# Kernel tuning notes

Measured on AMD Instinct MI355X. Metric: run time of the kernel, lower is better.

## Reference

```python
import jax, jax.numpy as jnp
import numpy as np

HID = 256      # hard-coded hidden_size in the torch module
LEVELS = 16    # topological levels in the generated DAG


def _lstm_cell(x, h, c, Wih, Whh, bih, bhh):
    # PyTorch LSTM cell: gates ordered (input, forget, cell, output)
    g = x @ Wih.T + h @ Whh.T + bih + bhh
    i, f, gg, o = jnp.split(g, 4, axis=-1)
    c_new = jax.nn.sigmoid(f) * c + jax.nn.sigmoid(i) * jnp.tanh(gg)
    h_new = jax.nn.sigmoid(o) * jnp.tanh(c_new)
    return h_new, c_new


def _forward(tokens, parents_idx, parent_valid,
             Wih_tok, Whh_tok, bih_tok, bhh_tok,
             Wih_ins, Whh_ins, bih_ins, bhh_ins, Wlin, blin):
    N, T, E = tokens.shape
    K = N // LEVELS
    NEG = jnp.asarray(-1e30, tokens.dtype)

    # --- token-level LSTM over each instruction's tokens, batched across instrs ---
    def tok_step(carry, x):
        h, c = carry
        return _lstm_cell(x, h, c, Wih_tok, Whh_tok, bih_tok, bhh_tok), None
    z = jnp.zeros((N, HID), tokens.dtype)
    (ins_embed, _), _ = jax.lax.scan(tok_step, (z, z), tokens.transpose(1, 0, 2))
    # ins_embed: [N, HID] = final token-LSTM hidden per instruction

    # --- instruction-level LSTM over the DAG, level by level ---
    H = jnp.zeros((N, HID), tokens.dtype)
    C = jnp.zeros((N, HID), tokens.dtype)
    for l in range(LEVELS):
        sl = slice(l * K, (l + 1) * K)
        pidx = parents_idx[sl]                 # [K, P] indices into earlier levels
        pval = parent_valid[sl][..., None]     # [K, P, 1]
        ph = jnp.where(pval, H[pidx], NEG).max(axis=1)   # max-reduction combine
        pc = jnp.where(pval, C[pidx], NEG).max(axis=1)
        has = parent_valid[sl].any(axis=1, keepdims=True)
        h0 = jnp.where(has, ph, 0.0)           # no parents -> zero init_hidden
        c0 = jnp.where(has, pc, 0.0)
        h1, c1 = _lstm_cell(ins_embed[sl], h0, c0, Wih_ins, Whh_ins, bih_ins, bhh_ins)
        H = H.at[sl].set(h1)
        C = C.at[sl].set(c1)

    # roots = instructions with no children (never referenced as a parent)
    appears = jnp.zeros((N,), jnp.int32).at[parents_idx.reshape(-1)].add(
        parent_valid.reshape(-1).astype(jnp.int32))
    root = (appears == 0)[:, None]
    final = jnp.where(root, H, NEG).max(axis=0)   # [HID]
    return final @ Wlin.T + blin                   # [num_classes]


def setup_inputs() -> dict:
    N, T, E, P = 2048, 16, 512, 8
    K = N // LEVELS
    rng = np.random.default_rng(0)
    pidx = np.zeros((N, P), np.int32)
    pval = np.zeros((N, P), bool)
    for l in range(1, LEVELS):
        pidx[l * K:(l + 1) * K] = rng.integers(0, l * K, (K, P))
        pval[l * K:(l + 1) * K] = rng.random((K, P)) < 0.75
    key = jax.random.key(0)
    ks = jax.random.split(key, 6)
    s = lambda k, shape, fan: jax.random.normal(k, shape, jnp.float32) / np.float32(np.sqrt(fan))
    return {
        "tokens": jax.random.normal(ks[0], (N, T, E), jnp.float32),
        "parents_idx": jnp.asarray(pidx),
        "parent_valid": jnp.asarray(pval),
        "Wih_tok": s(ks[1], (4 * HID, E), E),
        "Whh_tok": s(ks[2], (4 * HID, HID), HID),
        "bih_tok": jnp.zeros((4 * HID,), jnp.float32),
        "bhh_tok": jnp.zeros((4 * HID,), jnp.float32),
        "Wih_ins": s(ks[3], (4 * HID, HID), HID),
        "Whh_ins": s(ks[4], (4 * HID, HID), HID),
        "bih_ins": jnp.zeros((4 * HID,), jnp.float32),
        "bhh_ins": jnp.zeros((4 * HID,), jnp.float32),
        "Wlin": s(ks[5], (1, HID), HID),
        "blin": jnp.zeros((1,), jnp.float32),
    }


def reference(tokens, parents_idx, parent_valid,
              Wih_tok, Whh_tok, bih_tok, bhh_tok,
              Wih_ins, Whh_ins, bih_ins, bhh_ins, Wlin, blin):
    return _forward(tokens, parents_idx, parent_valid,
                    Wih_tok, Whh_tok, bih_tok, bhh_tok,
                    Wih_ins, Whh_ins, bih_ins, bhh_ins, Wlin, blin)
```

## Files before the change

### kernel.cpp

```cpp
#include <hip/hip_runtime.h>

#define NTOK 2048
#define TT   16
#define EE   512
#define HIDD 256
#define G4   1024
#define NLVL 16
#define KLVL 128
#define INV2048 (1.0f/2048.0f)

typedef _Float16 v8h __attribute__((ext_vector_type(8)));
typedef _Float16 v4h __attribute__((ext_vector_type(4)));
typedef float    v4f __attribute__((ext_vector_type(4)));

__device__ __forceinline__ v4f mfma16(v8h a, v8h b, v4f c) {
  return __builtin_amdgcn_mfma_f32_16x16x32_f16(a, b, c, 0, 0, 0);
}

__device__ __forceinline__ float fsig(float x) {
  return 1.0f / (1.0f + __expf(-x));
}
__device__ __forceinline__ float ftanh(float x) {
  float ax = fabsf(x);
  float e  = __expf(-2.0f * ax);
  float t  = (1.0f - e) / (1.0f + e);
  return copysignf(t, x);
}

__device__ __forceinline__ void split8(const v4f& w0, const v4f& w1, v8h& hi, v8h& lo) {
#pragma unroll
  for (int u = 0; u < 4; ++u) {
    float v = w0[u]; _Float16 h = (_Float16)v;
    hi[u] = h; lo[u] = (_Float16)((v - (float)h) * 2048.0f);
  }
#pragma unroll
  for (int u = 0; u < 4; ++u) {
    float v = w1[u]; _Float16 h = (_Float16)v;
    hi[4+u] = h; lo[4+u] = (_Float16)((v - (float)h) * 2048.0f);
  }
}

__device__ __forceinline__ v8h cvt8(const v4f& w0, const v4f& w1) {
  v8h r;
#pragma unroll
  for (int u = 0; u < 4; ++u) { r[u] = (_Float16)w0[u]; r[4+u] = (_Float16)w1[u]; }
  return r;
}

__global__ __launch_bounds__(256) void knorm(const void* __restrict__ pv_raw,
                                             unsigned char* __restrict__ pv8) {
  __shared__ int mode;
  const int tid = threadIdx.x;
  if (tid == 0) mode = 0;
  __syncthreads();
  const unsigned* pu = (const unsigned*)pv_raw;
  int local = 0;
  for (int i = tid; i < 4096; i += 256) {
    unsigned v = pu[i];
    if (v == 0x3F800000u) { local = 2; break; }
    if (v > 1u) local = 1;
  }
  if (local) atomicMax(&mode, local);
  __syncthreads();
  const int m = mode;
  const unsigned char* pb = (const unsigned char*)pv_raw;
  const float* pf = (const float*)pv_raw;
  const int* pi = (const int*)pv_raw;
  for (int i = tid; i < NTOK * 8; i += 256) {
    unsigned char v;
    if (m == 1)      v = (pb[i] != 0);
    else if (m == 2) v = (pf[i] != 0.0f);
    else             v = (pi[i] != 0);
    pv8[i] = v;
  }
}

__global__ __launch_bounds__(256) void kw_cvt(
    const float* __restrict__ a0, _Float16* __restrict__ f0,
    const float* __restrict__ a1, _Float16* __restrict__ f1,
    const float* __restrict__ a2, _Float16* __restrict__ f2,
    const float* __restrict__ a3, _Float16* __restrict__ f3) {
  const int t = blockIdx.x * 256 + threadIdx.x;
  if (t < 32768) {
    const int row = t >> 5, col8 = (t & 31) * 8;
    const int fc = row >> 4, l15 = row & 15;
    const int kk = col8 >> 5, lq = (col8 >> 3) & 3;
    const int lane8 = (lq * 16 + l15) * 8;
    const size_t srow = (size_t)row * 256 + col8;
    {
      v4f x0 = *(const v4f*)(a0 + srow), x1 = *(const v4f*)(a0 + srow + 4);
      *(v8h*)(f0 + (size_t)(fc * 8 + kk) * 512 + lane8) = cvt8(x0, x1);
    }
    {
      v4f x0 = *(const v4f*)(a1 + srow), x1 = *(const v4f*)(a1 + srow + 4);
      v8h hi, lo; split8(x0, x1, hi, lo);
      _Float16* d = f1 + (size_t)(fc * 8 + kk) * 1024 + lane8;
      *(v8h*)d = hi; *(v8h*)(d + 512) = lo;
    }
    {
      v4f x0 = *(const v4f*)(a2 + srow), x1 = *(const v4f*)(a2 + srow + 4);
      v8h hi, lo; split8(x0, x1, hi, lo);
      _Float16* d = f2 + (size_t)(fc * 8 + kk) * 1024 + lane8;
      *(v8h*)d = hi; *(v8h*)(d + 512) = lo;
    }
  } else {
    const int k = t - 32768;
    const int row = k >> 6, col8 = (k & 63) * 8;
    const int fc = row >> 4, l15 = row & 15;
    const int kk = col8 >> 5, lq = (col8 >> 3) & 3;
    const size_t srow = (size_t)row * 512 + col8;
    v4f x0 = *(const v4f*)(a3 + srow), x1 = *(const v4f*)(a3 + srow + 4);
    *(v8h*)(f3 + (size_t)(fc * 16 + kk) * 512 + (lq * 16 + l15) * 8) = cvt8(x0, x1);
  }
}

__global__ __launch_bounds__(512, 1) void kg2(const float* __restrict__ A,
                                              const _Float16* __restrict__ WtH,
                                              const float* __restrict__ b1,
                                              const float* __restrict__ b2,
                                              _Float16* __restrict__ Xg, int h) {
  __shared__ _Float16 As[64 * 520];
  const int tid  = threadIdx.x;
  const int lane = tid & 63;
  const int nq   = tid >> 6;
  const int l15  = lane & 15;
  const int lq   = lane >> 4;
  const int m0   = blockIdx.x * 64;

#pragma unroll
  for (int p = 0; p < 4; ++p) {
    const int row  = p * 16 + (tid >> 5);
    const int col0 = (tid & 31) * 16;
    const int ar   = m0 + row;
    const int tokrow = (ar & 2047) * 16 + h * 8 + (ar >> 11);
    const float* s = A + (size_t)tokrow * EE + col0;
    v4f x0 = *(const v4f*)s, x1 = *(const v4f*)(s + 4);
    v4f x2 = *(const v4f*)(s + 8), x3 = *(const v4f*)(s + 12);
    _Float16* d = As + row * 520 + col0;
    *(v8h*)d       = cvt8(x0, x1);
    *(v8h*)(d + 8) = cvt8(x2, x3);
  }
  __syncthreads();

  v4f acc[4][8];
#pragma unroll
  for (int n = 0; n < 8; ++n) {
    const int col = (nq * 8 + n) * 16 + l15;
    const float bb = b1[col] + b2[col];
#pragma unroll
    for (int m = 0; m < 4; ++m) acc[m][n] = (v4f){bb, bb, bb, bb};
  }

#pragma unroll 4
  for (int kk = 0; kk < 16; ++kk) {
    v8h af[4];
#pragma unroll
    for (int m = 0; m < 4; ++m)
      af[m] = *(const v8h*)(As + (m * 16 + l15) * 520 + kk * 32 + lq * 8);
#pragma unroll
    for (int n = 0; n < 8; ++n) {
      const int fc = nq * 8 + n;
      v8h bh = *(const v8h*)(WtH + (size_t)(fc * 16 + kk) * 512 + lane * 8);
#pragma unroll
      for (int m = 0; m < 4; ++m) acc[m][n] = mfma16(af[m], bh, acc[m][n]);
    }
  }

#pragma unroll
  for (int m = 0; m < 4; ++m)
#pragma unroll
    for (int n = 0; n < 8; ++n) {
      const int row = m0 + m * 16 + lq * 4;
      const int col = (nq * 8 + n) * 16 + l15;
      v4h o;
#pragma unroll
      for (int r = 0; r < 4; ++r) o[r] = (_Float16)acc[m][n][r];
      *(v4h*)(Xg + ((size_t)(row >> 2) * G4 + col) * 4) = o;
    }
}

__global__ __launch_bounds__(512, 1) void kr3(const _Float16* __restrict__ Xg,
                                              const _Float16* __restrict__ WhhH,
                                              float* __restrict__ Hst,
                                              float* __restrict__ Cst,
                                              _Float16* __restrict__ emb, int q) {
  __shared__ float hbuf[2][16 * 260];
  const int tid  = threadIdx.x;
  const int lane = tid & 63;
  const int w    = tid >> 6;
  const int wv   = w & 3;
  const int jh   = w >> 2;
  const int l15  = lane & 15;
  const int lq   = lane >> 4;
  const int r0   = blockIdx.x * 16;

  const _Float16* wbase = WhhH + (size_t)(8 * jh + wv) * 4096 + lane * 8;

  v4f c[2];
  if (q) {
#pragma unroll
    for (int j2 = 0; j2 < 2; ++j2) {
      const int feat = 16 * (wv + 4 * (2 * jh + j2)) + l15;
#pragma unroll
      for (int r = 0; r < 4; ++r)
        c[j2][r] = Cst[(size_t)(r0 + lq * 4 + r) * HIDD + feat];
    }
    for (int idx = tid; idx < 4096; idx += 512)
      hbuf[0][(idx >> 8) * 260 + (idx & 255)] = Hst[(size_t)(r0 + (idx >> 8)) * HIDD + (idx & 255)];
  } else {
    c[0] = (v4f){0.f, 0.f, 0.f, 0.f};
    c[1] = (v4f){0.f, 0.f, 0.f, 0.f};
  }

  v4h xp[4][2];
  {
    const size_t xrow = (size_t)((r0 >> 2) + lq) * G4;
#pragma unroll
    for (int g = 0; g < 4; ++g)
#pragma unroll
      for (int j2 = 0; j2 < 2; ++j2) {
        const int col = 256 * g + 16 * (wv + 4 * (2 * jh + j2)) + l15;
        xp[g][j2] = *(const v4h*)(Xg + (xrow + col) * 4);
      }
  }

  v8h bA[8], bB[8];
#pragma unroll
  for (int g = 0; g < 4; ++g)
#pragma unroll
    for (int j2 = 0; j2 < 2; ++j2)
      bA[g * 2 + j2] = *(const v8h*)(wbase + (16 * g + 4 * j2) * 4096);
  __syncthreads();

#pragma unroll 1
  for (int tl = 0; tl < 8; ++tl) {
    const int cur = tl & 1;
    const bool have_h = (q > 0) || (tl > 0);
    v4f acc[4][2];
#pragma unroll
    for (int g = 0; g < 4; ++g)
#pragma unroll
      for (int j2 = 0; j2 < 2; ++j2) {
        v4f a;
#pragma unroll
        for (int r = 0; r < 4; ++r) a[r] = (float)xp[g][j2][r];
        acc[g][j2] = a;
      }
    if (tl < 7) {
      const size_t xrow = (size_t)((tl + 1) * 512 + (r0 >> 2) + lq) * G4;
#pragma unroll
      for (int g = 0; g < 4; ++g)
#pragma unroll
        for (int j2 = 0; j2 < 2; ++j2) {
          const int col = 256 * g + 16 * (wv + 4 * (2 * jh + j2)) + l15;
          xp[g][j2] = *(const v4h*)(Xg + (xrow + col) * 4);
        }
    }
    if (have_h) {
#pragma unroll
      for (int kp = 0; kp < 4; ++kp) {
        const int k0 = 2 * kp, k1 = 2 * kp + 1;
#pragma unroll
        for (int g = 0; g < 4; ++g)
#pragma unroll
          for (int j2 = 0; j2 < 2; ++j2)
            bB[g * 2 + j2] = *(const v8h*)(wbase + (16 * g + 4 * j2) * 4096 + k1 * 512);
        {
          const int ko = k0 * 32 + lq * 8;
          v4f w0 = *(const v4f*)(hbuf[cur] + l15 * 260 + ko);
          v4f w1 = *(const v4f*)(hbuf[cur] + l15 * 260 + ko + 4);
          v8h ah = cvt8(w0, w1);
#pragma unroll
          for (int g = 0; g < 4; ++g)
#pragma unroll
            for (int j2 = 0; j2 < 2; ++j2)
              acc[g][j2] = mfma16(ah, bA[g * 2 + j2], acc[g][j2]);
        }
        if (kp < 3) {
#pragma unroll
          for (int g = 0; g < 4; ++g)
#pragma unroll
            for (int j2 = 0; j2 < 2; ++j2)
              bA[g * 2 + j2] = *(const v8h*)(wbase + (16 * g + 4 * j2) * 4096 + (k1 + 1) * 512);
        }
        {
          const int ko = k1 * 32 + lq * 8;
          v4f w0 = *(const v4f*)(hbuf[cur] + l15 * 260 + ko);
          v4f w1 = *(const v4f*)(hbuf[cur] + l15 * 260 + ko + 4);
          v8h ah = cvt8(w0, w1);
#pragma unroll
          for (int g = 0; g < 4; ++g)
#pragma unroll
            for (int j2 = 0; j2 < 2; ++j2)
              acc[g][j2] = mfma16(ah, bB[g * 2 + j2], acc[g][j2]);
        }
      }
      if (tl < 7) {
#pragma unroll
        for (int g = 0; g < 4; ++g)
#pragma unroll
          for (int j2 = 0; j2 < 2; ++j2)
            bA[g * 2 + j2] = *(const v8h*)(wbase + (16 * g + 4 * j2) * 4096);
      }
    }
#pragma unroll
    for (int j2 = 0; j2 < 2; ++j2) {
      const int feat = 16 * (wv + 4 * (2 * jh + j2)) + l15;
#pragma unroll
      for (int r = 0; r < 4; ++r) {
        const int rr = lq * 4 + r;
        float cn = fsig(acc[1][j2][r]) * c[j2][r] + fsig(acc[0][j2][r]) * ftanh(acc[2][j2][r]);
        float hn = fsig(acc[3][j2][r]) * ftanh(cn);
        c[j2][r] = cn;
        hbuf[cur ^ 1][rr * 260 + feat] = hn;
        if (tl == 7) {
          const size_t grow = r0 + rr;
          if (!q) { Hst[grow * HIDD + feat] = hn; Cst[grow * HIDD + feat] = cn; }
          else    { emb[grow * HIDD + feat] = (_Float16)hn; }
        }
      }
    }
    __syncthreads();
  }
}

__global__ __launch_bounds__(256) void kapp(const int* __restrict__ pidx,
                                            const unsigned char* __restrict__ pval,
                                            int* __restrict__ appears) {
  int e = blockIdx.x * 512 + threadIdx.x * 2;
#pragma unroll
  for (int u = 0; u < 2; ++u, ++e) {
    if (pval[e]) atomicAdd(appears + pidx[e], 1);
  }
}

__global__ __launch_bounds__(256) void klevel(
    const _Float16* __restrict__ emb,
    const _Float16* __restrict__ WihF, const _Float16* __restrict__ WhhF,
    const float* __restrict__ bi, const float* __restrict__ bh,
    const int* __restrict__ pidx, const unsigned char* __restrict__ pval,
    float* __restrict__ H, float* __restrict__ C, int l) {
  __shared__ _Float16 h0s[16 * 264];
  __shared__ float    c0s[16 * 68];
  __shared__ int      pis[128];
  __shared__ unsigned char pvs[128];
  const int tid  = threadIdx.x;
  const int lane = tid & 63;
  const int wv   = tid >> 6;
  const int l15  = lane & 15;
  const int lq   = lane >> 4;
  const int b    = blockIdx.x;
  const int mf   = b >> 2;
  const int q    = b & 3;
  const int fi   = q * 4 + wv;

  if (tid < 128) {
    int rr = tid >> 3, p = tid & 7;
    int row = l * KLVL + mf * 16 + rr;
    pis[tid] = pidx[row * 8 + p];
    pvs[tid] = pval[row * 8 + p];
  }
  __syncthreads();
#pragma unroll 1
  for (int it = 0; it < 4; ++it) {
    int task = tid + 256 * it;
    int rr = task >> 6;
    int f4 = (task & 63) * 4;
    v4f hm = (v4f){-1e30f, -1e30f, -1e30f, -1e30f};
    bool any = false;
#pragma unroll
    for (int p = 0; p < 8; ++p) {
      if (pvs[rr * 8 + p]) {
        any = true;
        v4f hv = *(const v4f*)(H + (size_t)pis[rr * 8 + p] * HIDD + f4);
#pragma unroll
        for (int u = 0; u < 4; ++u) hm[u] = fmaxf(hm[u], hv[u]);
      }
    }
    if (!any) hm = (v4f){0.f, 0.f, 0.f, 0.f};
    v4h h4;
#pragma unroll
    for (int u = 0; u < 4; ++u) h4[u] = (_Float16)hm[u];
    *(v4h*)(h0s + rr * 264 + f4) = h4;
  }
  {
    int rr = tid >> 4;
    int cc = (tid & 15) * 4;
    int f4 = q * 64 + cc;
    v4f cm = (v4f){-1e30f, -1e30f, -1e30f, -1e30f};
    bool any = false;
#pragma unroll
    for (int p = 0; p < 8; ++p) {
      if (pvs[rr * 8 + p]) {
        any = true;
        v4f cv = *(const v4f*)(C + (size_t)pis[rr * 8 + p] * HIDD + f4);
#pragma unroll
        for (int u = 0; u < 4; ++u) cm[u] = fmaxf(cm[u], cv[u]);
      }
    }
    if (!any) cm = (v4f){0.f, 0.f, 0.f, 0.f};
    *(v4f*)(c0s + rr * 68 + cc) = cm;
  }
  __syncthreads();

  v4f acc[4];
#pragma unroll
  for (int g = 0; g < 4; ++g) {
    int col  = 256 * g + 16 * fi + l15;
    float bb = bi[col] + bh[col];
    acc[g] = (v4f){bb, bb, bb, bb};
  }
  const int arow = l * KLVL + mf * 16 + l15;
#pragma unroll 1
  for (int kk = 0; kk < 8; ++kk) {
    const int ko = kk * 32 + lq * 8;
    v8h ax = *(const v8h*)(emb + (size_t)arow * HIDD + ko);
    v8h ah = *(const v8h*)(h0s + l15 * 264 + ko);
#pragma unroll
    for (int g = 0; g < 4; ++g) {
      const int fc = 16 * g + fi;
      acc[g] = mfma16(ax, *(const v8h*)(WihF + (size_t)(fc * 8 + kk) * 1024 + lane * 8), acc[g]);
      acc[g] = mfma16(ah, *(const v8h*)(WhhF + (size_t)(fc * 8 + kk) * 1024 + lane * 8), acc[g]);
    }
  }
#pragma unroll
  for (int r = 0; r < 4; ++r) {
    int rr = lq * 4 + r;
    int n  = 16 * fi + l15;
    float c0 = c0s[rr * 68 + 16 * wv + l15];
    float cn = fsig(acc[1][r]) * c0 + fsig(acc[0][r]) * ftanh(acc[2][r]);
    float hn = fsig(acc[3][r]) * ftanh(cn);
    int grow = l * KLVL + mf * 16 + rr;
    H[(size_t)grow * HIDD + n] = hn;
    C[(size_t)grow * HIDD + n] = cn;
  }
}

__global__ __launch_bounds__(256) void kroot1(const float* __restrict__ H,
                                              const int* __restrict__ appears,
                                              float* __restrict__ pmax) {
  __shared__ int app[64];
  const int tid = threadIdx.x;
  const int rb  = blockIdx.x * 64;
  if (tid < 64) app[tid] = appears[rb + tid];
  __syncthreads();
  float m = -1e30f;
#pragma unroll 1
  for (int r = 0; r < 64; ++r) {
    if (app[r] == 0) m = fmaxf(m, H[(size_t)(rb + r) * HIDD + tid]);
  }
  pmax[blockIdx.x * 256 + tid] = m;
}

__global__ __launch_bounds__(256) void kroot2(const float* __restrict__ pmax,
                                              const float* __restrict__ Wlin,
                                              const float* __restrict__ blin,
                                              float* __restrict__ out) {
  __shared__ float red[256];
  const int tid = threadIdx.x;
  float m = pmax[tid];
#pragma unroll 1
  for (int bb = 1; bb < 32; ++bb) m = fmaxf(m, pmax[bb * 256 + tid]);
  red[tid] = m * Wlin[tid];
  __syncthreads();
  if (tid == 0) {
    float s = 0.f;
    for (int i2 = 0; i2 < 256; ++i2) s += red[i2];
    out[0] = s + blin[0];
  }
}

extern "C" void kernel_launch(void* const* d_in, const int* in_sizes, int n_in,
                              void* d_out, int out_size, void* d_ws, size_t ws_size,
                              hipStream_t stream) {
  const float* tokens  = (const float*)d_in[0];
  const int*   pidx    = (const int*)d_in[1];
  const void*  pvraw   = (const void*)d_in[2];
  const float* Wih_tok = (const float*)d_in[3];
  const float* Whh_tok = (const float*)d_in[4];
  const float* bih_tok = (const float*)d_in[5];
  const float* bhh_tok = (const float*)d_in[6];
  const float* Wih_ins = (const float*)d_in[7];
  const float* Whh_ins = (const float*)d_in[8];
  const float* bih_ins = (const float*)d_in[9];
  const float* bhh_ins = (const float*)d_in[10];
  const float* Wlin    = (const float*)d_in[11];
  const float* blin    = (const float*)d_in[12];

  char* ws = (char*)d_ws;
  const size_t OFF_XG    = 0;
  const size_t OFF_H     = OFF_XG   + 33554432;
  const size_t OFF_C     = OFF_H    + 2097152;
  const size_t OFF_EMB   = OFF_C    + 2097152;
  const size_t OFF_WHHT  = OFF_EMB  + 1048576;
  const size_t OFF_WIHIF = OFF_WHHT + 524288;
  const size_t OFF_WHHIF = OFF_WIHIF + 1048576;
  const size_t OFF_WTH   = OFF_WHHIF + 1048576;
  const size_t OFF_APP   = OFF_WTH  + 1048576;
  const size_t OFF_PMX   = OFF_APP  + 8192;
  const size_t OFF_PV8   = OFF_PMX  + 32768;

  _Float16* Xg    = (_Float16*)(ws + OFF_XG);
  float*    Hbuf  = (float*)(ws + OFF_H);
  float*    Cbuf  = (float*)(ws + OFF_C);
  _Float16* emb   = (_Float16*)(ws + OFF_EMB);
  _Float16* WhhT  = (_Float16*)(ws + OFF_WHHT);
  _Float16* WihIF = (_Float16*)(ws + OFF_WIHIF);
  _Float16* WhhIF = (_Float16*)(ws + OFF_WHHIF);
  _Float16* WtH   = (_Float16*)(ws + OFF_WTH);
  int*      app   = (int*)(ws + OFF_APP);
  float*    pmx   = (float*)(ws + OFF_PMX);
  unsigned char* pv8 = (unsigned char*)(ws + OFF_PV8);

  hipMemsetAsync(ws + OFF_APP, 0, 8192, stream);

  knorm<<<dim3(1), dim3(256), 0, stream>>>(pvraw, pv8);
  kw_cvt<<<dim3(384), dim3(256), 0, stream>>>(Whh_tok, WhhT,
                                              Wih_ins, WihIF,
                                              Whh_ins, WhhIF,
                                              Wih_tok, WtH);
  kapp<<<dim3(32), dim3(256), 0, stream>>>(pidx, pv8, app);

  for (int h = 0; h < 2; ++h) {
    kg2<<<dim3(256), dim3(512), 0, stream>>>(tokens, WtH, bih_tok, bhh_tok, Xg, h);
    kr3<<<dim3(128), dim3(512), 0, stream>>>(Xg, WhhT, Hbuf, Cbuf, emb, h);
  }

  for (int l = 0; l < NLVL; ++l) {
    klevel<<<dim3(32), dim3(256), 0, stream>>>(emb, WihIF, WhhIF,
                                               bih_ins, bhh_ins, pidx, pv8,
                                               Hbuf, Cbuf, l);
  }
  kroot1<<<dim3(32), dim3(256), 0, stream>>>(Hbuf, app, pmx);
  kroot2<<<dim3(1), dim3(256), 0, stream>>>(pmx, Wlin, blin, (float*)d_out);
}
```

Before: 576.1 us.

## Hoist instruction-LSTM input projection into one GEMM; deepen weight prefetch in kr3

Adds a kernel that computes the input-to-gate projection for all instructions at once, with the biases folded in. It stores the result in an fp32 buffer in the MFMA output layout, so each of the 16 serial level kernels now runs only the recurrent half of the matmul and reads the precomputed gates. Separately, the token recurrence kernel now keeps three weight fragments in flight instead of one, using four rotating register buffers, to hide global-load latency behind the MFMAs. This costs an 8 MB scratch buffer, an extra launch, and higher register pressure in kr3.

```diff
diff --git a/kernel.cpp b/kernel.cpp
--- a/kernel.cpp
+++ b/kernel.cpp
@@ -179,6 +179,24 @@
     }
 }
 
+#define LOADB(BUF, KK)                                                         \
+  _Pragma("unroll")                                                            \
+  for (int g = 0; g < 4; ++g)                                                  \
+    _Pragma("unroll")                                                          \
+    for (int j2 = 0; j2 < 2; ++j2)                                             \
+      BUF[g * 2 + j2] = *(const v8h*)(wbase + (16 * g + 4 * j2) * 4096 + (KK) * 512);
+
+#define MFMAB(BUF, KK) {                                                       \
+  const int ko_ = (KK) * 32 + lq * 8;                                          \
+  v4f w0_ = *(const v4f*)(hb + l15 * 260 + ko_);                               \
+  v4f w1_ = *(const v4f*)(hb + l15 * 260 + ko_ + 4);                           \
+  v8h ah_ = cvt8(w0_, w1_);                                                    \
+  _Pragma("unroll")                                                            \
+  for (int g = 0; g < 4; ++g)                                                  \
+    _Pragma("unroll")                                                          \
+    for (int j2 = 0; j2 < 2; ++j2)                                             \
+      acc[g][j2] = mfma16(ah_, BUF[g * 2 + j2], acc[g][j2]); }
+
 __global__ __launch_bounds__(512, 1) void kr3(const _Float16* __restrict__ Xg,
                                               const _Float16* __restrict__ WhhH,
                                               float* __restrict__ Hst,
@@ -224,18 +242,15 @@
       }
   }
 
-  v8h bA[8], bB[8];
-#pragma unroll
-  for (int g = 0; g < 4; ++g)
-#pragma unroll
-    for (int j2 = 0; j2 < 2; ++j2)
-      bA[g * 2 + j2] = *(const v8h*)(wbase + (16 * g + 4 * j2) * 4096);
+  v8h b0[8], b1[8], b2[8], b3[8];
+  LOADB(b0, 0); LOADB(b1, 1); LOADB(b2, 2);
   __syncthreads();
 
 #pragma unroll 1
   for (int tl = 0; tl < 8; ++tl) {
     const int cur = tl & 1;
     const bool have_h = (q > 0) || (tl > 0);
+    const float* hb = hbuf[cur];
     v4f acc[4][2];
 #pragma unroll
     for (int g = 0; g < 4; ++g)
@@ -257,51 +272,15 @@
         }
     }
     if (have_h) {
-#pragma unroll
-      for (int kp = 0; kp < 4; ++kp) {
-        const int k0 = 2 * kp, k1 = 2 * kp + 1;
-#pragma unroll
-        for (int g = 0; g < 4; ++g)
-#pragma unroll
-          for (int j2 = 0; j2 < 2; ++j2)
-            bB[g * 2 + j2] = *(const v8h*)(wbase + (16 * g + 4 * j2) * 4096 + k1 * 512);
-        {
-          const int ko = k0 * 32 + lq * 8;
-          v4f w0 = *(const v4f*)(hbuf[cur] + l15 * 260 + ko);
-          v4f w1 = *(const v4f*)(hbuf[cur] + l15 * 260 + ko + 4);
-          v8h ah = cvt8(w0, w1);
-#pragma unroll
-          for (int g = 0; g < 4; ++g)
-#pragma unroll
-            for (int j2 = 0; j2 < 2; ++j2)
-              acc[g][j2] = mfma16(ah, bA[g * 2 + j2], acc[g][j2]);
-        }
-        if (kp < 3) {
-#pragma unroll
-          for (int g = 0; g < 4; ++g)
-#pragma unroll
-            for (int j2 = 0; j2 < 2; ++j2)
-              bA[g * 2 + j2] = *(const v8h*)(wbase + (16 * g + 4 * j2) * 4096 + (k1 + 1) * 512);
-        }
-        {
-          const int ko = k1 * 32 + lq * 8;
-          v4f w0 = *(const v4f*)(hbuf[cur] + l15 * 260 + ko);
-          v4f w1 = *(const v4f*)(hbuf[cur] + l15 * 260 + ko + 4);
-          v8h ah = cvt8(w0, w1);
-#pragma unroll
-          for (int g = 0; g < 4; ++g)
-#pragma unroll
-            for (int j2 = 0; j2 < 2; ++j2)
-              acc[g][j2] = mfma16(ah, bB[g * 2 + j2], acc[g][j2]);
-        }
-      }
-      if (tl < 7) {
-#pragma unroll
-        for (int g = 0; g < 4; ++g)
-#pragma unroll
-          for (int j2 = 0; j2 < 2; ++j2)
-            bA[g * 2 + j2] = *(const v8h*)(wbase + (16 * g + 4 * j2) * 4096);
-      }
+      LOADB(b3, 3); MFMAB(b0, 0);
+      LOADB(b0, 4); MFMAB(b1, 1);
+      LOADB(b1, 5); MFMAB(b2, 2);
+      LOADB(b2, 6); MFMAB(b3, 3);
+      LOADB(b3, 7); MFMAB(b0, 4);
+      MFMAB(b1, 5);
+      MFMAB(b2, 6);
+      MFMAB(b3, 7);
+      if (tl < 7) { LOADB(b0, 0); LOADB(b1, 1); LOADB(b2, 2); }
     }
 #pragma unroll
     for (int j2 = 0; j2 < 2; ++j2) {
@@ -324,6 +303,62 @@
   }
 }
 
+__global__ __launch_bounds__(512, 1) void kxi(const _Float16* __restrict__ emb,
+                                              const _Float16* __restrict__ WihF,
+                                              const float* __restrict__ bi,
+                                              const float* __restrict__ bh,
+                                              float* __restrict__ P) {
+  __shared__ _Float16 As[64 * 264];
+  const int tid  = threadIdx.x;
+  const int lane = tid & 63;
+  const int nq   = tid >> 6;
+  const int l15  = lane & 15;
+  const int lq   = lane >> 4;
+  const int m0   = blockIdx.x * 64;
+
+#pragma unroll
+  for (int p = 0; p < 4; ++p) {
+    const int idx = tid + 512 * p;
+    const int row = idx >> 5;
+    const int c8  = (idx & 31) * 8;
+    *(v8h*)(As + row * 264 + c8) = *(const v8h*)(emb + (size_t)(m0 + row) * HIDD + c8);
+  }
+  __syncthreads();
+
+  v4f acc[4][8];
+#pragma unroll
+  for (int n = 0; n < 8; ++n) {
+    const int col = (nq * 8 + n) * 16 + l15;
+    const float bb = bi[col] + bh[col];
+#pragma unroll
+    for (int m = 0; m < 4; ++m) acc[m][n] = (v4f){bb, bb, bb, bb};
+  }
+
+#pragma unroll 2
+  for (int kk = 0; kk < 8; ++kk) {
+    v8h af[4];
+#pragma unroll
+    for (int m = 0; m < 4; ++m)
+      af[m] = *(const v8h*)(As + (m * 16 + l15) * 264 + kk * 32 + lq * 8);
+#pragma unroll
+    for (int n = 0; n < 8; ++n) {
+      const int fc = nq * 8 + n;
+      v8h bhf = *(const v8h*)(WihF + (size_t)(fc * 8 + kk) * 1024 + lane * 8);
+#pragma unroll
+      for (int m = 0; m < 4; ++m) acc[m][n] = mfma16(af[m], bhf, acc[m][n]);
+    }
+  }
+
+#pragma unroll
+  for (int m = 0; m < 4; ++m)
+#pragma unroll
+    for (int n = 0; n < 8; ++n) {
+      const int row = m0 + m * 16 + lq * 4;
+      const int col = (nq * 8 + n) * 16 + l15;
+      *(v4f*)(P + ((size_t)(row >> 2) * G4 + col) * 4) = acc[m][n];
+    }
+}
+
 __global__ __launch_bounds__(256) void kapp(const int* __restrict__ pidx,
                                             const unsigned char* __restrict__ pval,
                                             int* __restrict__ appears) {
@@ -335,9 +370,8 @@
 }
 
 __global__ __launch_bounds__(256) void klevel(
-    const _Float16* __restrict__ emb,
-    const _Float16* __restrict__ WihF, const _Float16* __restrict__ WhhF,
-    const float* __restrict__ bi, const float* __restrict__ bh,
+    const float* __restrict__ P,
+    const _Float16* __restrict__ WhhF,
     const int* __restrict__ pidx, const unsigned char* __restrict__ pval,
     float* __restrict__ H, float* __restrict__ C, int l) {
   __shared__ _Float16 h0s[16 * 264];
@@ -404,22 +438,18 @@
   __syncthreads();
 
   v4f acc[4];
-#pragma unroll
-  for (int g = 0; g < 4; ++g) {
-    int col  = 256 * g + 16 * fi + l15;
-    float bb = bi[col] + bh[col];
-    acc[g] = (v4f){bb, bb, bb, bb};
-  }
-  const int arow = l * KLVL + mf * 16 + l15;
+  const int lrow4 = l * 32 + mf * 4 + lq;
+#pragma unroll
+  for (int g = 0; g < 4; ++g)
+    acc[g] = *(const v4f*)(P + ((size_t)lrow4 * G4 + 256 * g + 16 * fi + l15) * 4);
+
 #pragma unroll 1
   for (int kk = 0; kk < 8; ++kk) {
     const int ko = kk * 32 + lq * 8;
-    v8h ax = *(const v8h*)(emb + (size_t)arow * HIDD + ko);
     v8h ah = *(const v8h*)(h0s + l15 * 264 + ko);
 #pragma unroll
     for (int g = 0; g < 4; ++g) {
       const int fc = 16 * g + fi;
-      acc[g] = mfma16(ax, *(const v8h*)(WihF + (size_t)(fc * 8 + kk) * 1024 + lane * 8), acc[g]);
       acc[g] = mfma16(ah, *(const v8h*)(WhhF + (size_t)(fc * 8 + kk) * 1024 + lane * 8), acc[g]);
     }
   }
@@ -492,7 +522,8 @@
   const size_t OFF_H     = OFF_XG   + 33554432;
   const size_t OFF_C     = OFF_H    + 2097152;
   const size_t OFF_EMB   = OFF_C    + 2097152;
-  const size_t OFF_WHHT  = OFF_EMB  + 1048576;
+  const size_t OFF_P     = OFF_EMB  + 1048576;
+  const size_t OFF_WHHT  = OFF_P    + 8388608;
   const size_t OFF_WIHIF = OFF_WHHT + 524288;
   const size_t OFF_WHHIF = OFF_WIHIF + 1048576;
   const size_t OFF_WTH   = OFF_WHHIF + 1048576;
@@ -504,6 +535,7 @@
   float*    Hbuf  = (float*)(ws + OFF_H);
   float*    Cbuf  = (float*)(ws + OFF_C);
   _Float16* emb   = (_Float16*)(ws + OFF_EMB);
+  float*    Pbuf  = (float*)(ws + OFF_P);
   _Float16* WhhT  = (_Float16*)(ws + OFF_WHHT);
   _Float16* WihIF = (_Float16*)(ws + OFF_WIHIF);
   _Float16* WhhIF = (_Float16*)(ws + OFF_WHHIF);
@@ -526,9 +558,10 @@
     kr3<<<dim3(128), dim3(512), 0, stream>>>(Xg, WhhT, Hbuf, Cbuf, emb, h);
   }
 
+  kxi<<<dim3(32), dim3(512), 0, stream>>>(emb, WihIF, bih_ins, bhh_ins, Pbuf);
+
   for (int l = 0; l < NLVL; ++l) {
-    klevel<<<dim3(32), dim3(256), 0, stream>>>(emb, WihIF, WhhIF,
-                                               bih_ins, bhh_ins, pidx, pv8,
+    klevel<<<dim3(32), dim3(256), 0, stream>>>(Pbuf, WhhIF, pidx, pv8,
                                                Hbuf, Cbuf, l);
   }
   kroot1<<<dim3(32), dim3(256), 0, stream>>>(Hbuf, app, pmx);
```

New measurement: 599.9 us. +4.1%, slower.

## Precompute instruction-level input projection for all nodes before DAG level loop

Applied to the files above, without the earlier changes.

Moves the x@Wih^T + biases term of the instruction LSTM out of the 16 sequential per-level kernels into a single batched GEMM kernel over all 2048 instructions. The result is stored in an MFMA-fragment-ordered buffer so each level kernel loads its accumulator initialisation directly. This halves the MFMA work and weight traffic on the serial critical path. In exchange it adds one kernel launch and an 8 MB workspace buffer that is written once and read back.

```diff
diff --git a/kernel.cpp b/kernel.cpp
--- a/kernel.cpp
+++ b/kernel.cpp
@@ -324,6 +324,62 @@
   }
 }
 
+__global__ __launch_bounds__(512, 1) void kxi(const _Float16* __restrict__ emb,
+                                              const _Float16* __restrict__ WihF,
+                                              const float* __restrict__ bi,
+                                              const float* __restrict__ bh,
+                                              float* __restrict__ P) {
+  __shared__ _Float16 As[64 * 264];
+  const int tid  = threadIdx.x;
+  const int lane = tid & 63;
+  const int nq   = tid >> 6;
+  const int l15  = lane & 15;
+  const int lq   = lane >> 4;
+  const int m0   = blockIdx.x * 64;
+
+#pragma unroll
+  for (int p = 0; p < 4; ++p) {
+    const int idx = tid + 512 * p;
+    const int row = idx >> 5;
+    const int c8  = (idx & 31) * 8;
+    *(v8h*)(As + row * 264 + c8) = *(const v8h*)(emb + (size_t)(m0 + row) * HIDD + c8);
+  }
+  __syncthreads();
+
+  v4f acc[4][8];
+#pragma unroll
+  for (int n = 0; n < 8; ++n) {
+    const int col = (nq * 8 + n) * 16 + l15;
+    const float bb = bi[col] + bh[col];
+#pragma unroll
+    for (int m = 0; m < 4; ++m) acc[m][n] = (v4f){bb, bb, bb, bb};
+  }
+
+#pragma unroll 2
+  for (int kk = 0; kk < 8; ++kk) {
+    v8h af[4];
+#pragma unroll
+    for (int m = 0; m < 4; ++m)
+      af[m] = *(const v8h*)(As + (m * 16 + l15) * 264 + kk * 32 + lq * 8);
+#pragma unroll
+    for (int n = 0; n < 8; ++n) {
+      const int fc = nq * 8 + n;
+      v8h bhf = *(const v8h*)(WihF + (size_t)(fc * 8 + kk) * 1024 + lane * 8);
+#pragma unroll
+      for (int m = 0; m < 4; ++m) acc[m][n] = mfma16(af[m], bhf, acc[m][n]);
+    }
+  }
+
+#pragma unroll
+  for (int m = 0; m < 4; ++m)
+#pragma unroll
+    for (int n = 0; n < 8; ++n) {
+      const int row = m0 + m * 16 + lq * 4;
+      const int col = (nq * 8 + n) * 16 + l15;
+      *(v4f*)(P + ((size_t)(row >> 2) * G4 + col) * 4) = acc[m][n];
+    }
+}
+
 __global__ __launch_bounds__(256) void kapp(const int* __restrict__ pidx,
                                             const unsigned char* __restrict__ pval,
                                             int* __restrict__ appears) {
@@ -335,9 +391,8 @@
 }
 
 __global__ __launch_bounds__(256) void klevel(
-    const _Float16* __restrict__ emb,
-    const _Float16* __restrict__ WihF, const _Float16* __restrict__ WhhF,
-    const float* __restrict__ bi, const float* __restrict__ bh,
+    const float* __restrict__ P,
+    const _Float16* __restrict__ WhhF,
     const int* __restrict__ pidx, const unsigned char* __restrict__ pval,
     float* __restrict__ H, float* __restrict__ C, int l) {
   __shared__ _Float16 h0s[16 * 264];
@@ -404,22 +459,18 @@
   __syncthreads();
 
   v4f acc[4];
-#pragma unroll
-  for (int g = 0; g < 4; ++g) {
-    int col  = 256 * g + 16 * fi + l15;
-    float bb = bi[col] + bh[col];
-    acc[g] = (v4f){bb, bb, bb, bb};
-  }
-  const int arow = l * KLVL + mf * 16 + l15;
+  const int lrow4 = l * 32 + mf * 4 + lq;
+#pragma unroll
+  for (int g = 0; g < 4; ++g)
+    acc[g] = *(const v4f*)(P + ((size_t)lrow4 * G4 + 256 * g + 16 * fi + l15) * 4);
+
 #pragma unroll 1
   for (int kk = 0; kk < 8; ++kk) {
     const int ko = kk * 32 + lq * 8;
-    v8h ax = *(const v8h*)(emb + (size_t)arow * HIDD + ko);
     v8h ah = *(const v8h*)(h0s + l15 * 264 + ko);
 #pragma unroll
     for (int g = 0; g < 4; ++g) {
       const int fc = 16 * g + fi;
-      acc[g] = mfma16(ax, *(const v8h*)(WihF + (size_t)(fc * 8 + kk) * 1024 + lane * 8), acc[g]);
       acc[g] = mfma16(ah, *(const v8h*)(WhhF + (size_t)(fc * 8 + kk) * 1024 + lane * 8), acc[g]);
     }
   }
@@ -492,7 +543,8 @@
   const size_t OFF_H     = OFF_XG   + 33554432;
   const size_t OFF_C     = OFF_H    + 2097152;
   const size_t OFF_EMB   = OFF_C    + 2097152;
-  const size_t OFF_WHHT  = OFF_EMB  + 1048576;
+  const size_t OFF_P     = OFF_EMB  + 1048576;
+  const size_t OFF_WHHT  = OFF_P    + 8388608;
   const size_t OFF_WIHIF = OFF_WHHT + 524288;
   const size_t OFF_WHHIF = OFF_WIHIF + 1048576;
   const size_t OFF_WTH   = OFF_WHHIF + 1048576;
@@ -504,6 +556,7 @@
   float*    Hbuf  = (float*)(ws + OFF_H);
   float*    Cbuf  = (float*)(ws + OFF_C);
   _Float16* emb   = (_Float16*)(ws + OFF_EMB);
+  float*    Pbuf  = (float*)(ws + OFF_P);
   _Float16* WhhT  = (_Float16*)(ws + OFF_WHHT);
   _Float16* WihIF = (_Float16*)(ws + OFF_WIHIF);
   _Float16* WhhIF = (_Float16*)(ws + OFF_WHHIF);
@@ -526,9 +579,10 @@
     kr3<<<dim3(128), dim3(512), 0, stream>>>(Xg, WhhT, Hbuf, Cbuf, emb, h);
   }
 
+  kxi<<<dim3(32), dim3(512), 0, stream>>>(emb, WihIF, bih_ins, bhh_ins, Pbuf);
+
   for (int l = 0; l < NLVL; ++l) {
-    klevel<<<dim3(32), dim3(256), 0, stream>>>(emb, WihIF, WhhIF,
-                                               bih_ins, bhh_ins, pidx, pv8,
+    klevel<<<dim3(32), dim3(256), 0, stream>>>(Pbuf, WhhIF, pidx, pv8,
                                                Hbuf, Cbuf, l);
   }
   kroot1<<<dim3(32), dim3(256), 0, stream>>>(Hbuf, app, pmx);
```

New measurement: 494.3 us, median of 2. 1.17x faster.
